# Performance work log

Hardware: AMD Instinct MI355X
Metric: run time of the kernel (lower is better)

Reference implementation:

```python
import jax, jax.numpy as jnp
import numpy as np

NUM_CHARS = 26  # hardcoded in original module


def setup_inputs() -> dict:
    key = jax.random.key(0)
    ks = jax.random.split(key, 8)
    B, T, H = 2048, 1024, NUM_CHARS
    s = 1.0 / np.sqrt(H)
    return {
        "x": jax.random.randint(ks[0], (B, T), 0, NUM_CHARS, dtype=jnp.int64),
        "E": jax.random.normal(ks[1], (NUM_CHARS, H), dtype=jnp.float32),            # embedding table
        "W_ih": jax.random.uniform(ks[2], (4 * H, H), jnp.float32, -s, s),           # LSTM input weights (i,f,g,o)
        "W_hh": jax.random.uniform(ks[3], (4 * H, H), jnp.float32, -s, s),           # LSTM hidden weights
        "b_ih": jax.random.uniform(ks[4], (4 * H,), jnp.float32, -s, s),
        "b_hh": jax.random.uniform(ks[5], (4 * H,), jnp.float32, -s, s),
        "W_lin": jax.random.uniform(ks[6], (NUM_CHARS, H), jnp.float32, -s, s),      # final Linear weight
        "b_lin": jax.random.uniform(ks[7], (NUM_CHARS,), jnp.float32, -s, s),
    }


def reference(x, E, W_ih, W_hh, b_ih, b_hh, W_lin, b_lin):
    # Embedding lookup: [B,T] -> [B,T,H]
    emb = E[x]
    B, T, H = emb.shape
    # Precompute input projections for all timesteps: [B,T,4H]
    x_proj = jnp.einsum('bth,gh->btg', emb, W_ih) + b_ih

    def step(carry, xt):  # xt: [B,4H]
        h, c = carry
        gates = xt + h @ W_hh.T + b_hh  # [B,4H], torch gate order i,f,g,o
        i, f, g, o = jnp.split(gates, 4, axis=-1)
        i = jax.nn.sigmoid(i)
        f = jax.nn.sigmoid(f)
        g = jnp.tanh(g)
        o = jax.nn.sigmoid(o)
        c = f * c + i * g
        h = o * jnp.tanh(c)
        return (h, c), None

    h0 = jnp.zeros((B, H), emb.dtype)
    (hT, _), _ = jax.lax.scan(step, (h0, h0), jnp.swapaxes(x_proj, 0, 1))
    # h_n has shape [num_layers=1, B, H]; .squeeze(1) is a no-op for B>1
    out = hT @ W_lin.T + b_lin  # [B,26]
    return out[None]  # [1,B,26]
```

## Files before the change

### kernel.cpp

```cpp
#include <hip/hip_runtime.h>

#define LOG2E 1.442695040888963f

__launch_bounds__(64, 2)
__global__ void lstm_char_kernel(const int* __restrict__ x,
                                 const float* __restrict__ E,
                                 const float* __restrict__ W_ih,
                                 const float* __restrict__ W_hh,
                                 const float* __restrict__ b_ih,
                                 const float* __restrict__ b_hh,
                                 const float* __restrict__ W_lin,
                                 const float* __restrict__ b_lin,
                                 float* __restrict__ out,
                                 int T)
{
    constexpr int H = 26;

    __shared__ float P[27][104];
    __shared__ float Ebuf[26 * 26];
    __shared__ int   chars[1024 + 2];
    __shared__ __align__(16) float hbuf[64];

    const int b = blockIdx.x;
    const int l = threadIdx.x;
    const bool act = (l < 52);
    const int r0 = act ? l : 0;
    const int r1 = act ? l + 52 : 0;

    for (int i = l; i < 26 * 26; i += 64) Ebuf[i] = E[i];
    for (int t = l; t < T; t += 64) chars[t] = x[(size_t)b * T + t] * (104 * 4);
    if (l < 2) chars[T + l] = 0;
    hbuf[l] = 0.0f;

    float wh0[H], wh1[H];
    {
        float wi0[H], wi1[H];
        #pragma unroll
        for (int k = 0; k < H; ++k) {
            wi0[k] = W_ih[r0 * H + k];
            wh0[k] = W_hh[r0 * H + k];
            wi1[k] = W_ih[r1 * H + k];
            wh1[k] = W_hh[r1 * H + k];
        }
        const float bias0 = b_ih[r0] + b_hh[r0];
        const float bias1 = b_ih[r1] + b_hh[r1];
        __syncthreads();

        for (int ch = 0; ch < 26; ++ch) {
            float a0 = bias0, a1 = bias1;
            #pragma unroll
            for (int k = 0; k < H; ++k) {
                float e = Ebuf[ch * H + k];
                a0 = fmaf(wi0[k], e, a0);
                a1 = fmaf(wi1[k], e, a1);
            }
            if (act) { P[ch][l] = a0; P[ch][52 + l] = a1; }
        }
    }
    __syncthreads();

    const float m1 = (l < 26) ? (-2.0f * LOG2E) : (-LOG2E);
    const float s1 = (l < 26) ? 2.0f : 1.0f;
    const float d1 = (l < 26) ? -1.0f : 0.0f;
    const int bpaddr = ((l + 26) & 63) << 2;

    int poff0 = chars[0];
    int poffn = chars[1];
    const char* Pbase = (const char*)&P[0][0];
    const float* Pr0 = (const float*)(Pbase + poff0);
    float pa0 = Pr0[l];
    float pa1 = Pr0[l + 52];

    float c = 0.0f;

    #pragma unroll 2
    for (int t = 0; t < T; ++t) {
        const float* Pn = (const float*)(Pbase + poffn);
        float pn0 = Pn[l];
        float pn1 = Pn[l + 52];
        int poff2 = chars[t + 2];

        float hr[28];
        #pragma unroll
        for (int q = 0; q < 7; ++q) {
            float4 v = ((const float4*)hbuf)[q];
            hr[4 * q + 0] = v.x; hr[4 * q + 1] = v.y;
            hr[4 * q + 2] = v.z; hr[4 * q + 3] = v.w;
        }

        float s00 = pa0, s01 = 0.0f, s10 = pa1, s11 = 0.0f;
        #pragma unroll
        for (int k = 0; k < H; k += 2) {
            s00 = fmaf(wh0[k],     hr[k],     s00);
            s01 = fmaf(wh0[k + 1], hr[k + 1], s01);
            s10 = fmaf(wh1[k],     hr[k],     s10);
            s11 = fmaf(wh1[k + 1], hr[k + 1], s11);
        }
        const float a0 = s00 + s01;
        const float a1 = s10 + s11;

        float y0 = __builtin_amdgcn_rcpf(1.0f + __builtin_amdgcn_exp2f(a0 * (-LOG2E)));
        float y1 = fmaf(__builtin_amdgcn_rcpf(1.0f + __builtin_amdgcn_exp2f(a1 * m1)),
                        s1, d1);

        float fg = __int_as_float(__builtin_amdgcn_ds_bpermute(bpaddr, __float_as_int(y0)));
        float og = __int_as_float(__builtin_amdgcn_ds_bpermute(bpaddr, __float_as_int(y1)));

        c = fmaf(fg, c, y0 * y1);
        float th = fmaf(__builtin_amdgcn_rcpf(
                            1.0f + __builtin_amdgcn_exp2f(c * (-2.0f * LOG2E))),
                        2.0f, -1.0f);
        hbuf[l] = og * th;

        pa0 = pn0; pa1 = pn1; poffn = poff2;
    }

    __syncthreads();

    if (l < H) {
        float acc = b_lin[l];
        #pragma unroll
        for (int k = 0; k < H; ++k)
            acc = fmaf(W_lin[l * H + k], hbuf[k], acc);
        out[(size_t)b * H + l] = acc;
    }
}

extern "C" void kernel_launch(void* const* d_in, const int* in_sizes, int n_in,
                              void* d_out, int out_size, void* d_ws, size_t ws_size,
                              hipStream_t stream) {
    const int*   x     = (const int*)d_in[0];
    const float* E     = (const float*)d_in[1];
    const float* W_ih  = (const float*)d_in[2];
    const float* W_hh  = (const float*)d_in[3];
    const float* b_ih  = (const float*)d_in[4];
    const float* b_hh  = (const float*)d_in[5];
    const float* W_lin = (const float*)d_in[6];
    const float* b_lin = (const float*)d_in[7];
    float* out = (float*)d_out;

    const int T = 1024;
    const int B = in_sizes[0] / T;

    lstm_char_kernel<<<B, 64, 0, stream>>>(x, E, W_ih, W_hh, b_ih, b_hh,
                                           W_lin, b_lin, out, T);
}
```

Before: 288.5 us.

## Interleave two batch sequences per wavefront and fold gate scaling into weights

Each 64-thread block now runs two independent batch rows, interleaving their LSTM steps so one sequence's LDS round-trip and transcendental latency overlap with the other's FMA chain. The -log2e scale factors are folded into W_hh and the precomputed input projections, removing per-step multiplies. The gate-exchange permutes are cut from two to one by permuting the i*g product and writing h to a shifted index. The grid is halved, which leaves fewer waves to spread across the GPU's compute units.

```diff
diff --git a/kernel.cpp b/kernel.cpp
--- a/kernel.cpp
+++ b/kernel.cpp
@@ -2,7 +2,7 @@
 
 #define LOG2E 1.442695040888963f
 
-__launch_bounds__(64, 2)
+__launch_bounds__(64, 1)
 __global__ void lstm_char_kernel(const int* __restrict__ x,
                                  const float* __restrict__ E,
                                  const float* __restrict__ W_ih,
@@ -17,20 +17,32 @@
     constexpr int H = 26;
 
     __shared__ float P[27][104];
-    __shared__ float Ebuf[26 * 26];
-    __shared__ int   chars[1024 + 2];
-    __shared__ __align__(16) float hbuf[64];
+    __shared__ float Ebuf[676];
+    __shared__ int   chars0[1026];
+    __shared__ int   chars1[1026];
+    __shared__ __align__(16) float hbuf0[64];
+    __shared__ __align__(16) float hbuf1[64];
 
-    const int b = blockIdx.x;
     const int l = threadIdx.x;
+    const size_t b0 = 2 * (size_t)blockIdx.x;
+    const size_t b1 = b0 + 1;
     const bool act = (l < 52);
     const int r0 = act ? l : 0;
     const int r1 = act ? l + 52 : 0;
 
-    for (int i = l; i < 26 * 26; i += 64) Ebuf[i] = E[i];
-    for (int t = l; t < T; t += 64) chars[t] = x[(size_t)b * T + t] * (104 * 4);
-    if (l < 2) chars[T + l] = 0;
-    hbuf[l] = 0.0f;
+    for (int i = l; i < 676; i += 64) Ebuf[i] = E[i];
+    for (int t = l; t < T; t += 64) {
+        chars0[t] = x[b0 * T + t] * 416;
+        chars1[t] = x[b1 * T + t] * 416;
+    }
+    if (l < 2) { chars0[1024 + l] = 0; chars1[1024 + l] = 0; }
+    hbuf0[l] = 0.0f;
+    hbuf1[l] = 0.0f;
+
+    const float m0 = -LOG2E;
+    const float m1 = (l < 26) ? (-2.0f * LOG2E) : (-LOG2E);
+    const float s1 = (l < 26) ? 2.0f : 1.0f;
+    const float d1 = (l < 26) ? -1.0f : 0.0f;
 
     float wh0[H], wh1[H];
     {
@@ -38,14 +50,13 @@
         #pragma unroll
         for (int k = 0; k < H; ++k) {
             wi0[k] = W_ih[r0 * H + k];
-            wh0[k] = W_hh[r0 * H + k];
             wi1[k] = W_ih[r1 * H + k];
-            wh1[k] = W_hh[r1 * H + k];
+            wh0[k] = W_hh[r0 * H + k] * m0;
+            wh1[k] = W_hh[r1 * H + k] * m1;
         }
         const float bias0 = b_ih[r0] + b_hh[r0];
         const float bias1 = b_ih[r1] + b_hh[r1];
         __syncthreads();
-
         for (int ch = 0; ch < 26; ++ch) {
             float a0 = bias0, a1 = bias1;
             #pragma unroll
@@ -54,75 +65,113 @@
                 a0 = fmaf(wi0[k], e, a0);
                 a1 = fmaf(wi1[k], e, a1);
             }
-            if (act) { P[ch][l] = a0; P[ch][52 + l] = a1; }
+            if (act) { P[ch][l] = a0 * m0; P[ch][52 + l] = a1 * m1; }
         }
     }
     __syncthreads();
 
-    const float m1 = (l < 26) ? (-2.0f * LOG2E) : (-LOG2E);
-    const float s1 = (l < 26) ? 2.0f : 1.0f;
-    const float d1 = (l < 26) ? -1.0f : 0.0f;
-    const int bpaddr = ((l + 26) & 63) << 2;
+    const int bpaddr = ((l - 26) & 63) << 2;
+    const int hidx   = (l - 26) & 63;
 
-    int poff0 = chars[0];
-    int poffn = chars[1];
-    const char* Pbase = (const char*)&P[0][0];
-    const float* Pr0 = (const float*)(Pbase + poff0);
-    float pa0 = Pr0[l];
-    float pa1 = Pr0[l + 52];
+    const char* Pb = (const char*)&P[0][0];
+    int pf0 = chars0[1];
+    int pf1 = chars1[1];
+    float pa00, pa01, pa10, pa11;
+    { const float* r = (const float*)(Pb + chars0[0]); pa00 = r[l]; pa01 = r[l + 52]; }
+    { const float* r = (const float*)(Pb + chars1[0]); pa10 = r[l]; pa11 = r[l + 52]; }
+    float c0 = 0.0f, c1 = 0.0f;
 
-    float c = 0.0f;
+    float hr0[28];
+    #pragma unroll
+    for (int q = 0; q < 7; ++q) {
+        float4 v = ((const float4*)hbuf0)[q];
+        hr0[4*q] = v.x; hr0[4*q+1] = v.y; hr0[4*q+2] = v.z; hr0[4*q+3] = v.w;
+    }
 
-    #pragma unroll 2
     for (int t = 0; t < T; ++t) {
-        const float* Pn = (const float*)(Pbase + poffn);
-        float pn0 = Pn[l];
-        float pn1 = Pn[l + 52];
-        int poff2 = chars[t + 2];
-
-        float hr[28];
+        float hr1[28];
         #pragma unroll
         for (int q = 0; q < 7; ++q) {
-            float4 v = ((const float4*)hbuf)[q];
-            hr[4 * q + 0] = v.x; hr[4 * q + 1] = v.y;
-            hr[4 * q + 2] = v.z; hr[4 * q + 3] = v.w;
+            float4 v = ((const float4*)hbuf1)[q];
+            hr1[4*q] = v.x; hr1[4*q+1] = v.y; hr1[4*q+2] = v.z; hr1[4*q+3] = v.w;
+        }
+        const float* Pn0 = (const float*)(Pb + pf0);
+        const float* Pn1 = (const float*)(Pb + pf1);
+        float q00 = Pn0[l], q01 = Pn0[l + 52];
+        float q10 = Pn1[l], q11 = Pn1[l + 52];
+        int pf0n = chars0[t + 2];
+        int pf1n = chars1[t + 2];
+
+        {
+            float u0 = pa00, u1 = 0.0f, u2 = pa01, u3 = 0.0f;
+            #pragma unroll
+            for (int k = 0; k < H; k += 2) {
+                u0 = fmaf(wh0[k],     hr0[k],     u0);
+                u1 = fmaf(wh0[k + 1], hr0[k + 1], u1);
+                u2 = fmaf(wh1[k],     hr0[k],     u2);
+                u3 = fmaf(wh1[k + 1], hr0[k + 1], u3);
+            }
+            const float a0 = u0 + u1;
+            const float a1 = u2 + u3;
+            float y0 = __builtin_amdgcn_rcpf(1.0f + __builtin_amdgcn_exp2f(a0));
+            float y1 = fmaf(__builtin_amdgcn_rcpf(1.0f + __builtin_amdgcn_exp2f(a1)),
+                            s1, d1);
+            float pr = y0 * y1;
+            float pp = __int_as_float(
+                __builtin_amdgcn_ds_bpermute(bpaddr, __float_as_int(pr)));
+            c0 = fmaf(y0, c0, pp);
+            float th = fmaf(__builtin_amdgcn_rcpf(
+                                1.0f + __builtin_amdgcn_exp2f(c0 * (-2.0f * LOG2E))),
+                            2.0f, -1.0f);
+            hbuf0[hidx] = y1 * th;
         }
 
-        float s00 = pa0, s01 = 0.0f, s10 = pa1, s11 = 0.0f;
         #pragma unroll
-        for (int k = 0; k < H; k += 2) {
-            s00 = fmaf(wh0[k],     hr[k],     s00);
-            s01 = fmaf(wh0[k + 1], hr[k + 1], s01);
-            s10 = fmaf(wh1[k],     hr[k],     s10);
-            s11 = fmaf(wh1[k + 1], hr[k + 1], s11);
+        for (int q = 0; q < 7; ++q) {
+            float4 v = ((const float4*)hbuf0)[q];
+            hr0[4*q] = v.x; hr0[4*q+1] = v.y; hr0[4*q+2] = v.z; hr0[4*q+3] = v.w;
         }
-        const float a0 = s00 + s01;
-        const float a1 = s10 + s11;
 
-        float y0 = __builtin_amdgcn_rcpf(1.0f + __builtin_amdgcn_exp2f(a0 * (-LOG2E)));
-        float y1 = fmaf(__builtin_amdgcn_rcpf(1.0f + __builtin_amdgcn_exp2f(a1 * m1)),
-                        s1, d1);
+        {
+            float u0 = pa10, u1 = 0.0f, u2 = pa11, u3 = 0.0f;
+            #pragma unroll
+            for (int k = 0; k < H; k += 2) {
+                u0 = fmaf(wh0[k],     hr1[k],     u0);
+                u1 = fmaf(wh0[k + 1], hr1[k + 1], u1);
+                u2 = fmaf(wh1[k],     hr1[k],     u2);
+                u3 = fmaf(wh1[k + 1], hr1[k + 1], u3);
+            }
+            const float a0 = u0 + u1;
+            const float a1 = u2 + u3;
+            float y0 = __builtin_amdgcn_rcpf(1.0f + __builtin_amdgcn_exp2f(a0));
+            float y1 = fmaf(__builtin_amdgcn_rcpf(1.0f + __builtin_amdgcn_exp2f(a1)),
+                            s1, d1);
+            float pr = y0 * y1;
+            float pp = __int_as_float(
+                __builtin_amdgcn_ds_bpermute(bpaddr, __float_as_int(pr)));
+            c1 = fmaf(y0, c1, pp);
+            float th = fmaf(__builtin_amdgcn_rcpf(
+                                1.0f + __builtin_amdgcn_exp2f(c1 * (-2.0f * LOG2E))),
+                            2.0f, -1.0f);
+            hbuf1[hidx] = y1 * th;
+        }
 
-        float fg = __int_as_float(__builtin_amdgcn_ds_bpermute(bpaddr, __float_as_int(y0)));
-        float og = __int_as_float(__builtin_amdgcn_ds_bpermute(bpaddr, __float_as_int(y1)));
-
-        c = fmaf(fg, c, y0 * y1);
-        float th = fmaf(__builtin_amdgcn_rcpf(
-                            1.0f + __builtin_amdgcn_exp2f(c * (-2.0f * LOG2E))),
-                        2.0f, -1.0f);
-        hbuf[l] = og * th;
-
-        pa0 = pn0; pa1 = pn1; poffn = poff2;
+        pa00 = q00; pa01 = q01; pa10 = q10; pa11 = q11;
+        pf0 = pf0n; pf1 = pf1n;
     }
 
     __syncthreads();
 
     if (l < H) {
-        float acc = b_lin[l];
+        float acc0 = b_lin[l], acc1 = b_lin[l];
         #pragma unroll
-        for (int k = 0; k < H; ++k)
-            acc = fmaf(W_lin[l * H + k], hbuf[k], acc);
-        out[(size_t)b * H + l] = acc;
+        for (int k = 0; k < H; ++k) {
+            float w = W_lin[l * H + k];
+            acc0 = fmaf(w, hbuf0[k], acc0);
+            acc1 = fmaf(w, hbuf1[k], acc1);
+        }
+        out[b0 * H + l] = acc0;
+        out[b1 * H + l] = acc1;
     }
 }
 
@@ -142,6 +191,6 @@
     const int T = 1024;
     const int B = in_sizes[0] / T;
 
-    lstm_char_kernel<<<B, 64, 0, stream>>>(x, E, W_ih, W_hh, b_ih, b_hh,
-                                           W_lin, b_lin, out, T);
+    lstm_char_kernel<<<B / 2, 64, 0, stream>>>(x, E, W_ih, W_hh, b_ih, b_hh,
+                                               W_lin, b_lin, out, T);
 }
```

New measurement: 446.6 us. 54.8% more time.

## Use packed FP32 FMAs, prescaled weights, and single bpermute in LSTM step

Applied to the files above, without the earlier changes.

The recurrent weights and the precomputed input projections are scaled ahead of time by the exp2 multipliers, which removes a multiply per gate on the critical path. The hidden-state matvec now uses v_pk_fma_f32 on float pairs, and the P table is interleaved as float2 so one 8-byte load fetches both gate rows. Lane ownership is remapped so that only the i*g product needs a single ds_bpermute per step, where two were used before, and h is written to a shifted index. Risks include inline asm that blocks compiler scheduling and changed rounding order.

```diff
diff --git a/kernel.cpp b/kernel.cpp
--- a/kernel.cpp
+++ b/kernel.cpp
@@ -1,6 +1,16 @@
 #include <hip/hip_runtime.h>
 
 #define LOG2E 1.442695040888963f
+
+typedef float f32x2 __attribute__((ext_vector_type(2)));
+typedef float f32x4 __attribute__((ext_vector_type(4)));
+
+static __device__ __forceinline__ void pkfma(f32x2& acc, f32x2 a, f32x2 b) {
+    asm("v_pk_fma_f32 %0, %1, %2, %0" : "+v"(acc) : "v"(a), "v"(b));
+}
+static __device__ __forceinline__ void pkmul(f32x2& d, f32x2 a, f32x2 b) {
+    asm("v_pk_mul_f32 %0, %1, %2" : "=v"(d) : "v"(a), "v"(b));
+}
 
 __launch_bounds__(64, 2)
 __global__ void lstm_char_kernel(const int* __restrict__ x,
@@ -16,9 +26,9 @@
 {
     constexpr int H = 26;
 
-    __shared__ float P[27][104];
-    __shared__ float Ebuf[26 * 26];
-    __shared__ int   chars[1024 + 2];
+    __shared__ __align__(16) f32x2 P[27][52];
+    __shared__ float Ebuf[676];
+    __shared__ int   chars[1026];
     __shared__ __align__(16) float hbuf[64];
 
     const int b = blockIdx.x;
@@ -27,25 +37,33 @@
     const int r0 = act ? l : 0;
     const int r1 = act ? l + 52 : 0;
 
-    for (int i = l; i < 26 * 26; i += 64) Ebuf[i] = E[i];
-    for (int t = l; t < T; t += 64) chars[t] = x[(size_t)b * T + t] * (104 * 4);
-    if (l < 2) chars[T + l] = 0;
+    for (int i = l; i < 676; i += 64) Ebuf[i] = E[i];
+    for (int t = l; t < T; t += 64) chars[t] = x[(size_t)b * T + t] * 416;
+    if (l < 2) chars[1024 + l] = 0;
     hbuf[l] = 0.0f;
 
-    float wh0[H], wh1[H];
+    const float m0 = -LOG2E;
+    const float m1 = (l < 26) ? (-2.0f * LOG2E) : (-LOG2E);
+    const float s1 = (l < 26) ? 2.0f : 1.0f;
+    const float d1 = (l < 26) ? -1.0f : 0.0f;
+
+    f32x2 wh0p[13], wh1p[13];
+    #pragma unroll
+    for (int k = 0; k < 13; ++k) {
+        wh0p[k] = f32x2{W_hh[r0 * H + 2 * k] * m0, W_hh[r0 * H + 2 * k + 1] * m0};
+        wh1p[k] = f32x2{W_hh[r1 * H + 2 * k] * m1, W_hh[r1 * H + 2 * k + 1] * m1};
+    }
+
     {
         float wi0[H], wi1[H];
         #pragma unroll
         for (int k = 0; k < H; ++k) {
             wi0[k] = W_ih[r0 * H + k];
-            wh0[k] = W_hh[r0 * H + k];
             wi1[k] = W_ih[r1 * H + k];
-            wh1[k] = W_hh[r1 * H + k];
         }
         const float bias0 = b_ih[r0] + b_hh[r0];
         const float bias1 = b_ih[r1] + b_hh[r1];
         __syncthreads();
-
         for (int ch = 0; ch < 26; ++ch) {
             float a0 = bias0, a1 = bias1;
             #pragma unroll
@@ -54,65 +72,63 @@
                 a0 = fmaf(wi0[k], e, a0);
                 a1 = fmaf(wi1[k], e, a1);
             }
-            if (act) { P[ch][l] = a0; P[ch][52 + l] = a1; }
+            if (act) P[ch][l] = f32x2{a0 * m0, a1 * m1};
         }
     }
     __syncthreads();
 
-    const float m1 = (l < 26) ? (-2.0f * LOG2E) : (-LOG2E);
-    const float s1 = (l < 26) ? 2.0f : 1.0f;
-    const float d1 = (l < 26) ? -1.0f : 0.0f;
-    const int bpaddr = ((l + 26) & 63) << 2;
+    const int bpaddr = ((l - 26) & 63) << 2;
+    const int hidx   = (l - 26) & 63;
+    const char* Pb = (const char*)&P[0][0];
+    const int lane8 = l << 3;
 
-    int poff0 = chars[0];
     int poffn = chars[1];
-    const char* Pbase = (const char*)&P[0][0];
-    const float* Pr0 = (const float*)(Pbase + poff0);
-    float pa0 = Pr0[l];
-    float pa1 = Pr0[l + 52];
-
+    f32x2 pa = *(const f32x2*)(Pb + chars[0] + lane8);
     float c = 0.0f;
 
     #pragma unroll 2
     for (int t = 0; t < T; ++t) {
-        const float* Pn = (const float*)(Pbase + poffn);
-        float pn0 = Pn[l];
-        float pn1 = Pn[l + 52];
+        f32x2 hp[13];
+        #pragma unroll
+        for (int q = 0; q < 13; ++q) hp[q] = ((const f32x2*)hbuf)[q];
+
+        f32x2 pn = *(const f32x2*)(Pb + poffn + lane8);
         int poff2 = chars[t + 2];
 
-        float hr[28];
+        f32x2 A0, A1, B0, B1;
+        pkmul(A0, wh0p[0], hp[0]);
+        pkmul(A1, wh0p[1], hp[1]);
+        pkmul(B0, wh1p[0], hp[0]);
+        pkmul(B1, wh1p[1], hp[1]);
         #pragma unroll
-        for (int q = 0; q < 7; ++q) {
-            float4 v = ((const float4*)hbuf)[q];
-            hr[4 * q + 0] = v.x; hr[4 * q + 1] = v.y;
-            hr[4 * q + 2] = v.z; hr[4 * q + 3] = v.w;
+        for (int k = 2; k < 12; k += 2) {
+            pkfma(A0, wh0p[k],     hp[k]);
+            pkfma(A1, wh0p[k + 1], hp[k + 1]);
+            pkfma(B0, wh1p[k],     hp[k]);
+            pkfma(B1, wh1p[k + 1], hp[k + 1]);
         }
+        pkfma(A0, wh0p[12], hp[12]);
+        pkfma(B0, wh1p[12], hp[12]);
+        f32x2 sa = A0 + A1;
+        f32x2 sb = B0 + B1;
+        const float a0s = sa.x + sa.y + pa.x;
+        const float a1s = sb.x + sb.y + pa.y;
 
-        float s00 = pa0, s01 = 0.0f, s10 = pa1, s11 = 0.0f;
-        #pragma unroll
-        for (int k = 0; k < H; k += 2) {
-            s00 = fmaf(wh0[k],     hr[k],     s00);
-            s01 = fmaf(wh0[k + 1], hr[k + 1], s01);
-            s10 = fmaf(wh1[k],     hr[k],     s10);
-            s11 = fmaf(wh1[k + 1], hr[k + 1], s11);
-        }
-        const float a0 = s00 + s01;
-        const float a1 = s10 + s11;
-
-        float y0 = __builtin_amdgcn_rcpf(1.0f + __builtin_amdgcn_exp2f(a0 * (-LOG2E)));
-        float y1 = fmaf(__builtin_amdgcn_rcpf(1.0f + __builtin_amdgcn_exp2f(a1 * m1)),
+        float y0 = __builtin_amdgcn_rcpf(1.0f + __builtin_amdgcn_exp2f(a0s));
+        float y1 = fmaf(__builtin_amdgcn_rcpf(1.0f + __builtin_amdgcn_exp2f(a1s)),
                         s1, d1);
 
-        float fg = __int_as_float(__builtin_amdgcn_ds_bpermute(bpaddr, __float_as_int(y0)));
-        float og = __int_as_float(__builtin_amdgcn_ds_bpermute(bpaddr, __float_as_int(y1)));
+        float pr = y0 * y1;
+        float pp = __int_as_float(
+            __builtin_amdgcn_ds_bpermute(bpaddr, __float_as_int(pr)));
 
-        c = fmaf(fg, c, y0 * y1);
+        c = fmaf(y0, c, pp);
         float th = fmaf(__builtin_amdgcn_rcpf(
                             1.0f + __builtin_amdgcn_exp2f(c * (-2.0f * LOG2E))),
                         2.0f, -1.0f);
-        hbuf[l] = og * th;
+        hbuf[hidx] = y1 * th;
 
-        pa0 = pn0; pa1 = pn1; poffn = poff2;
+        pa = pn; poffn = poff2;
     }
 
     __syncthreads();
```

Result: faster. 282.3 us (-2.2%).
